# Performance work log

Measured on AMD Instinct MI355X. Metric: run time of the kernel, lower is better.

## Reference

```python
import jax, jax.numpy as jnp
import numpy as np

NUM_HEADS = 16
HIDDEN = 1024
HEAD_DIM = HIDDEN // NUM_HEADS


def setup_inputs() -> dict:
    key = jax.random.key(0)
    ks = jax.random.split(key, 12)
    B, S, H = 4, 1024, HIDDEN
    s = 1.0 / np.sqrt(H)
    inp = {
        "aspect_hidden": jax.random.normal(ks[0], (B, S, H), jnp.float32),
        "opinion_hidden": jax.random.normal(ks[1], (B, S, H), jnp.float32),
        "attention_mask": jnp.ones((B, S), jnp.int32),
        # torch nn.Linear weights are [out, in]
        "Wq": jax.random.normal(ks[2], (H, H), jnp.float32) * s,
        "bq": jnp.zeros((H,), jnp.float32),
        "Wk": jax.random.normal(ks[3], (H, H), jnp.float32) * s,
        "bk": jnp.zeros((H,), jnp.float32),
        "Wv": jax.random.normal(ks[4], (H, H), jnp.float32) * s,
        "bv": jnp.zeros((H,), jnp.float32),
        "Wo": jax.random.normal(ks[5], (H, H), jnp.float32) * s,
        "bo": jnp.zeros((H,), jnp.float32),
        # nn.Bilinear(H, H, 1): weight [1, H, H], bias [1]
        "Wbil": jax.random.normal(ks[6], (1, H, H), jnp.float32) * s,
        "bbil": jnp.zeros((1,), jnp.float32),
    }
    return inp


def reference(aspect_hidden, opinion_hidden, attention_mask,
              Wq, bq, Wk, bk, Wv, bv, Wo, bo, Wbil, bbil):
    B, Sq, H = aspect_hidden.shape
    Sk = opinion_hidden.shape[1]
    nh, hd = NUM_HEADS, HEAD_DIM
    scale = hd ** (-0.5)

    q = (aspect_hidden @ Wq.T + bq).reshape(B, Sq, nh, hd).transpose(0, 2, 1, 3)
    k = (opinion_hidden @ Wk.T + bk).reshape(B, Sk, nh, hd).transpose(0, 2, 1, 3)
    v = (opinion_hidden @ Wv.T + bv).reshape(B, Sk, nh, hd).transpose(0, 2, 1, 3)

    # bilinear span bias: span[b,s] = a[b,s] @ Wbil[0] @ o[b,s] + bbil
    span = jnp.einsum('bsh,hk,bsk->bs', aspect_hidden, Wbil[0], opinion_hidden) + bbil[0]

    # scores [B, nh, Sq, Sk] with span bias broadcast over heads and keys
    scores = jnp.einsum('bhqd,bhkd->bhqk', q, k) * scale + span[:, None, :, None]
    scores = jnp.where(attention_mask[:, None, None, :] == 0, -jnp.inf, scores)

    probs = jax.nn.softmax(scores, axis=-1)
    ctx = jnp.einsum('bhqk,bhkd->bhqd', probs, v)
    ctx = ctx.transpose(0, 2, 1, 3).reshape(B, Sq, H)
    return ctx @ Wo.T + bo
```

## Files before the change

kernel.cpp:

```cpp
#include <hip/hip_runtime.h>
#include <hip/hip_bf16.h>
#include <stdint.h>

typedef __attribute__((ext_vector_type(4))) float f32x4;
typedef __attribute__((ext_vector_type(16))) float f32x16;
typedef __attribute__((ext_vector_type(8))) short bf16x8;
typedef __attribute__((ext_vector_type(4))) unsigned int u32x4;
typedef __attribute__((ext_vector_type(2))) unsigned int u32x2;
typedef unsigned short u16;

#define GBL_AS1(p) ((const __attribute__((address_space(1))) void*)(p))
#define LDS_AS3(p) ((__attribute__((address_space(3))) void*)(p))

static __device__ __forceinline__ u16 f2bf(float f) {
  __hip_bfloat16 h = __float2bfloat16(f);
  union { __hip_bfloat16 h; u16 u; } c; c.h = h;
  return c.u;
}

__global__ __launch_bounds__(256) void fused_cast(
    const float* __restrict__ a, const float* __restrict__ o,
    const float* __restrict__ wq_, const float* __restrict__ wk_,
    const float* __restrict__ wv_, const float* __restrict__ wo_,
    const int* __restrict__ mask,
    u16* __restrict__ aB, u16* __restrict__ oB,
    u16* __restrict__ WqB, u16* __restrict__ WkB,
    u16* __restrict__ WvB, u16* __restrict__ WoB,
    int* __restrict__ flags) {
  if (blockIdx.x == 0 && threadIdx.x < 64) {
    int bb = threadIdx.x >> 4, kt = threadIdx.x & 15;
    int anyz = 0;
    for (int s = 0; s < 64; ++s) anyz |= (mask[bb * 1024 + kt * 64 + s] == 0);
    flags[threadIdx.x] = anyz;
  }
  int idx = blockIdx.x * 256 + threadIdx.x;
#pragma unroll
  for (int j = 0; j < 4; ++j) {
    int i = idx + j * 786432;
    const float* src; u16* dst; int off;
    if (i < 1048576) { src = a; dst = aB; off = i; }
    else if (i < 2097152) { src = o; dst = oB; off = i - 1048576; }
    else {
      int w = (i - 2097152) >> 18; off = (i - 2097152) & 262143;
      src = (w == 0) ? wq_ : (w == 1) ? wk_ : (w == 2) ? wv_ : wo_;
      dst = (w == 0) ? WqB : (w == 1) ? WkB : (w == 2) ? WvB : WoB;
    }
    float4 v = reinterpret_cast<const float4*>(src)[off];
    ushort4 ov;
    ov.x = f2bf(v.x); ov.y = f2bf(v.y); ov.z = f2bf(v.z); ov.w = f2bf(v.w);
    reinterpret_cast<ushort4*>(dst)[off] = ov;
  }
}

static __device__ __forceinline__ void gemm_core(const u16* __restrict__ Atile,
                                                 const u16* __restrict__ Btile,
                                                 u16* lds_a, u16* lds_b,
                                                 f32x4 acc[4][4]) {
  const int tid = threadIdx.x;
  const int lane = tid & 63;
  const int wv = tid >> 6;
  const int wm = wv >> 1, wn = wv & 1;
  const int fr = lane & 15, fq = lane >> 4;
  for (int kt = 0; kt < 32; ++kt) {
#pragma unroll
    for (int i = 0; i < 2; ++i) {
      const int cb = (wv * 2 + i) * 64;
      const int c = cb + lane;
      const int row = c >> 2;
      const int off = (c & 3) * 8;
      __builtin_amdgcn_global_load_lds(GBL_AS1(Atile + (size_t)row * 1024 + kt * 32 + off),
                                       LDS_AS3(lds_a + cb * 8), 16, 0, 0);
      __builtin_amdgcn_global_load_lds(GBL_AS1(Btile + (size_t)row * 1024 + kt * 32 + off),
                                       LDS_AS3(lds_b + cb * 8), 16, 0, 0);
    }
    __syncthreads();
    bf16x8 af[4], bfv[4];
#pragma unroll
    for (int mi = 0; mi < 4; ++mi)
      af[mi] = *(const bf16x8*)&lds_a[(wm * 64 + mi * 16 + fr) * 32 + fq * 8];
#pragma unroll
    for (int ni = 0; ni < 4; ++ni)
      bfv[ni] = *(const bf16x8*)&lds_b[(wn * 64 + ni * 16 + fr) * 32 + fq * 8];
#pragma unroll
    for (int mi = 0; mi < 4; ++mi)
#pragma unroll
      for (int ni = 0; ni < 4; ++ni)
        acc[mi][ni] = __builtin_amdgcn_mfma_f32_16x16x32_bf16(af[mi], bfv[ni], acc[mi][ni], 0, 0, 0);
    __syncthreads();
  }
}

__global__ __launch_bounds__(256) void qkv_gemm(
    const u16* __restrict__ aB, const u16* __restrict__ oB,
    const u16* __restrict__ Wq, const u16* __restrict__ Wk, const u16* __restrict__ Wv,
    const float* __restrict__ bq, const float* __restrict__ bk, const float* __restrict__ bv,
    u16* __restrict__ q_ws, u16* __restrict__ k_ws, u16* __restrict__ vt_ws) {
  __shared__ __align__(16) u16 lds_a[128 * 32];
  __shared__ __align__(16) u16 lds_b[128 * 32];
  const int mt = blockIdx.x;
  const int nt = blockIdx.y;
  const int w = nt >> 3, ntl = nt & 7;
  const u16* A = (w == 0) ? aB : oB;
  const u16* W = (w == 0) ? Wq : (w == 1) ? Wk : Wv;
  const float* bias = (w == 0) ? bq : (w == 1) ? bk : bv;
  f32x4 acc[4][4];
#pragma unroll
  for (int i = 0; i < 4; ++i)
#pragma unroll
    for (int j = 0; j < 4; ++j) acc[i][j] = (f32x4){0.f, 0.f, 0.f, 0.f};
  gemm_core(A + (size_t)mt * 128 * 1024, W + (size_t)ntl * 128 * 1024, lds_a, lds_b, acc);
  const int lane = threadIdx.x & 63, wvi = threadIdx.x >> 6;
  const int wm = wvi >> 1, wn = wvi & 1, fr = lane & 15, fq = lane >> 4;
  u16* dst01 = (w == 0) ? q_ws : k_ws;
  const float qscl = (w == 0) ? 0.18033688f : 1.0f;
#pragma unroll
  for (int mi = 0; mi < 4; ++mi)
#pragma unroll
    for (int ni = 0; ni < 4; ++ni)
#pragma unroll
      for (int r = 0; r < 4; ++r) {
        int m = mt * 128 + wm * 64 + mi * 16 + fq * 4 + r;
        int nl = ntl * 128 + wn * 64 + ni * 16 + fr;
        float v = (acc[mi][ni][r] + bias[nl]) * qscl;
        int b = m >> 10, s = m & 1023, h = nl >> 6, d = nl & 63;
        u16 u = f2bf(v);
        if (w < 2) dst01[(((size_t)(b * 16 + h)) * 1024 + s) * 64 + d] = u;
        else       vt_ws[(((size_t)(b * 16 + h)) * 64 + d) * 1024 + s] = u;
      }
}

__global__ __launch_bounds__(256, 4) void attn_kernel(
    const u16* __restrict__ q_ws, const u16* __restrict__ k_ws,
    const u16* __restrict__ vt_ws, const int* __restrict__ mask,
    const int* __restrict__ flags, u16* __restrict__ ctx_ws) {
  __shared__ __align__(16) u16 k_lds[2][64 * 64];
  __shared__ __align__(16) u16 vt_lds[2][64 * 64];
  __shared__ __align__(16) float scl_lds[4][32];
  const int bid = blockIdx.x;
  const int bh = bid & 63, qt = bid >> 6;
  const int b = bh >> 4, h = bh & 15;
  const int tid = threadIdx.x, lane = tid & 63, wv = tid >> 6;
  const int l31 = lane & 31, hi = lane >> 5;
  const u16* qbase = q_ws + (size_t)bh * 65536 + (size_t)qt * 8192;
  const u16* kbase = k_ws + (size_t)bh * 65536;
  const u16* vtbase = vt_ws + (size_t)bh * 65536;

#define STAGE_KV(kt_, buf_) do { \
    _Pragma("unroll") \
    for (int i_ = 0; i_ < 2; ++i_) { \
      int cb_ = (wv * 2 + i_) * 64; \
      int c_ = cb_ + lane; \
      int r_ = c_ >> 3; \
      int sc_ = ((c_ & 7) ^ (r_ & 7)) * 8; \
      __builtin_amdgcn_global_load_lds(GBL_AS1(kbase + (size_t)((kt_) * 64 + r_) * 64 + sc_), \
                                       LDS_AS3(&k_lds[buf_][cb_ * 8]), 16, 0, 0); \
      __builtin_amdgcn_global_load_lds(GBL_AS1(vtbase + (size_t)r_ * 1024 + (kt_) * 64 + sc_), \
                                       LDS_AS3(&vt_lds[buf_][cb_ * 8]), 16, 0, 0); \
    } \
  } while (0)

  {
    u16* qstage = &k_lds[0][0];
#pragma unroll
    for (int i_ = 0; i_ < 4; ++i_) {
      int cb_ = (wv * 4 + i_) * 64;
      int c_ = cb_ + lane;
      int r_ = c_ >> 3;
      int sc_ = ((c_ & 7) ^ (r_ & 7)) * 8;
      __builtin_amdgcn_global_load_lds(GBL_AS1(qbase + (size_t)r_ * 64 + sc_),
                                       LDS_AS3(qstage + cb_ * 8), 16, 0, 0);
    }
  }
  __syncthreads();
  bf16x8 qf[4];
  {
    int rq = wv * 32 + l31;
    const u16* qr = &k_lds[0][0] + rq * 64;
    int rx = rq & 7;
#pragma unroll
    for (int ds = 0; ds < 4; ++ds)
      qf[ds] = *(const bf16x8*)&qr[((ds * 2 + hi) ^ rx) * 8];
  }
  __syncthreads();
  STAGE_KV(0, 0);
  __syncthreads();

  f32x16 ctx0, ctx1;
#pragma unroll
  for (int z = 0; z < 16; ++z) { ctx0[z] = 0.f; ctx1[z] = 0.f; }
  float psum_half = 0.f;

  for (int kt = 0; kt < 16; ++kt) {
    const int cur = kt & 1;
    if (kt < 15) STAGE_KV(kt + 1, cur ^ 1);

    f32x16 sc[2];
#pragma unroll
    for (int kb = 0; kb < 2; ++kb) {
      f32x16 a;
#pragma unroll
      for (int z = 0; z < 16; ++z) a[z] = 0.f;
      int r = kb * 32 + l31;
      const u16* kr = &k_lds[cur][r * 64];
      int rx = r & 7;
#pragma unroll
      for (int ds = 0; ds < 4; ++ds) {
        bf16x8 kf = *(const bf16x8*)&kr[((ds * 2 + hi) ^ rx) * 8];
        a = __builtin_amdgcn_mfma_f32_32x32x16_bf16(kf, qf[ds], a, 0, 0, 0);
      }
      sc[kb] = a;
    }

    if (flags[b * 16 + kt]) {
#pragma unroll
      for (int kb = 0; kb < 2; ++kb)
#pragma unroll
        for (int r2 = 0; r2 < 16; ++r2) {
          int key = kb * 32 + (r2 & 3) + 8 * (r2 >> 2) + 4 * hi;
          if (mask[b * 1024 + kt * 64 + key] == 0) sc[kb][r2] = -30000.0f;
        }
    }

#pragma unroll
    for (int kb = 0; kb < 2; ++kb)
#pragma unroll
      for (int r2 = 0; r2 < 16; ++r2) {
        float p = __builtin_exp2f(sc[kb][r2]);
        sc[kb][r2] = p;
        psum_half += p;
      }

#pragma unroll
    for (int kb = 0; kb < 2; ++kb) {
      unsigned int w[8];
#pragma unroll
      for (int j = 0; j < 8; ++j) {
        unsigned int t;
        asm("v_cvt_pk_bf16_f32 %0, %1, %2" : "=v"(t) : "v"(sc[kb][2 * j]), "v"(sc[kb][2 * j + 1]));
        w[j] = t;
      }
      u32x2 a0 = __builtin_amdgcn_permlane32_swap(w[0], w[2], false, false);
      u32x2 a1 = __builtin_amdgcn_permlane32_swap(w[1], w[3], false, false);
      u32x2 a2 = __builtin_amdgcn_permlane32_swap(w[4], w[6], false, false);
      u32x2 a3 = __builtin_amdgcn_permlane32_swap(w[5], w[7], false, false);
      union { u32x4 u; bf16x8 b; } P0, P1;
      P0.u = (u32x4){ a0[0], a1[0], a0[1], a1[1] };
      P1.u = (u32x4){ a2[0], a3[0], a2[1], a3[1] };
#pragma unroll
      for (int db = 0; db < 2; ++db) {
        int rv = db * 32 + l31;
        const u16* vr = &vt_lds[cur][rv * 64];
        int rvx = rv & 7;
        bf16x8 v0 = *(const bf16x8*)&vr[((kb * 4 + hi) ^ rvx) * 8];
        bf16x8 v1 = *(const bf16x8*)&vr[((kb * 4 + 2 + hi) ^ rvx) * 8];
        if (db == 0) {
          ctx0 = __builtin_amdgcn_mfma_f32_32x32x16_bf16(P0.b, v0, ctx0, 0, 0, 0);
          ctx0 = __builtin_amdgcn_mfma_f32_32x32x16_bf16(P1.b, v1, ctx0, 0, 0, 0);
        } else {
          ctx1 = __builtin_amdgcn_mfma_f32_32x32x16_bf16(P0.b, v0, ctx1, 0, 0, 0);
          ctx1 = __builtin_amdgcn_mfma_f32_32x32x16_bf16(P1.b, v1, ctx1, 0, 0, 0);
        }
      }
    }
    __syncthreads();
  }

  float lrow = psum_half + __shfl_xor(psum_half, 32);
  float inv = (lrow > 0.f) ? 1.0f / lrow : 0.f;
  if (hi == 0) scl_lds[wv][l31] = inv;
  asm volatile("s_waitcnt lgkmcnt(0)" ::: "memory");
  const int sbase = qt * 128 + wv * 32;
#pragma unroll
  for (int g = 0; g < 4; ++g) {
    float4 s4 = *(const float4*)&scl_lds[wv][g * 8 + hi * 4];
    const float* sp = (const float*)&s4;
#pragma unroll
    for (int i2 = 0; i2 < 4; ++i2) {
      int s = sbase + g * 8 + hi * 4 + i2;
      size_t rowoff = ((size_t)(b * 1024 + s)) * 1024 + h * 64;
      ctx_ws[rowoff + l31]      = f2bf(ctx0[g * 4 + i2] * sp[i2]);
      ctx_ws[rowoff + 32 + l31] = f2bf(ctx1[g * 4 + i2] * sp[i2]);
    }
  }
#undef STAGE_KV
}

__global__ __launch_bounds__(256) void out_gemm(const u16* __restrict__ ctxB,
                                                const u16* __restrict__ Wo,
                                                const float* __restrict__ bo,
                                                float* __restrict__ out) {
  __shared__ __align__(16) u16 lds_a[128 * 32];
  __shared__ __align__(16) u16 lds_b[128 * 32];
  const int mt = blockIdx.x, nt = blockIdx.y;
  f32x4 acc[4][4];
#pragma unroll
  for (int i = 0; i < 4; ++i)
#pragma unroll
    for (int j = 0; j < 4; ++j) acc[i][j] = (f32x4){0.f, 0.f, 0.f, 0.f};
  gemm_core(ctxB + (size_t)mt * 128 * 1024, Wo + (size_t)nt * 128 * 1024, lds_a, lds_b, acc);
  const int lane = threadIdx.x & 63, wvi = threadIdx.x >> 6;
  const int wm = wvi >> 1, wn = wvi & 1, fr = lane & 15, fq = lane >> 4;
#pragma unroll
  for (int mi = 0; mi < 4; ++mi)
#pragma unroll
    for (int ni = 0; ni < 4; ++ni)
#pragma unroll
      for (int r = 0; r < 4; ++r) {
        int m = mt * 128 + wm * 64 + mi * 16 + fq * 4 + r;
        int n = nt * 128 + wn * 64 + ni * 16 + fr;
        out[(size_t)m * 1024 + n] = acc[mi][ni][r] + bo[n];
      }
}

extern "C" void kernel_launch(void* const* d_in, const int* in_sizes, int n_in,
                              void* d_out, int out_size, void* d_ws, size_t ws_size,
                              hipStream_t stream) {
  const float* aspect = (const float*)d_in[0];
  const float* opinion = (const float*)d_in[1];
  const int* mask = (const int*)d_in[2];
  const float* Wq = (const float*)d_in[3];
  const float* bq = (const float*)d_in[4];
  const float* Wk = (const float*)d_in[5];
  const float* bk = (const float*)d_in[6];
  const float* Wv = (const float*)d_in[7];
  const float* bv = (const float*)d_in[8];
  const float* Wo = (const float*)d_in[9];
  const float* bo = (const float*)d_in[10];
  float* out = (float*)d_out;
  char* ws = (char*)d_ws;

  const size_t MB = 1u << 20;
  u16* aB    = (u16*)(ws + 0 * MB);
  u16* oB    = (u16*)(ws + 8 * MB);
  u16* WqB   = (u16*)(ws + 16 * MB);
  u16* WkB   = (u16*)(ws + 18 * MB);
  u16* WvB   = (u16*)(ws + 20 * MB);
  u16* WoB   = (u16*)(ws + 22 * MB);
  u16* q_ws  = (u16*)(ws + 24 * MB);
  u16* k_ws  = (u16*)(ws + 32 * MB);
  u16* vt_ws = (u16*)(ws + 40 * MB);
  u16* ctx_ws= (u16*)(ws + 48 * MB);
  int* flags = (int*)(out + out_size - 64);

  fused_cast<<<3072, 256, 0, stream>>>(aspect, opinion, Wq, Wk, Wv, Wo, mask,
                                       aB, oB, WqB, WkB, WvB, WoB, flags);
  qkv_gemm<<<dim3(32, 24), 256, 0, stream>>>(aB, oB, WqB, WkB, WvB, bq, bk, bv,
                                             q_ws, k_ws, vt_ws);
  attn_kernel<<<512, 256, 0, stream>>>(q_ws, k_ws, vt_ws, mask, flags, ctx_ws);
  out_gemm<<<dim3(32, 8), 256, 0, stream>>>(ctx_ws, WoB, bo, out);
}
```

Before: 109.4 us.

## Double-buffer GEMM LDS staging, remap blocks for XCD locality, vectorize V^T stores

The shared GEMM core now uses two LDS buffers and issues the global-to-LDS loads for the next k-step before computing on the current one, so memory latency overlaps the MFMA work. The QKV and output GEMMs switch to a 1D grid with an index remap that spreads consecutive block IDs across the 8 XCDs, so blocks sharing tiles run on the same XCD and can reuse its L2. The V-transpose epilogue writes four consecutive sequence positions as one ushort4 store instead of scattered 2-byte stores. The cost is doubled LDS per block (32KB) and only one barrier per iteration between the compute and the next overwrite.

```diff
diff --git a/kernel.cpp b/kernel.cpp
--- a/kernel.cpp
+++ b/kernel.cpp
@@ -61,26 +61,35 @@
   const int wv = tid >> 6;
   const int wm = wv >> 1, wn = wv & 1;
   const int fr = lane & 15, fq = lane >> 4;
+
+#define GSTAGE(kt_, buf_) do { \
+    _Pragma("unroll") \
+    for (int i_ = 0; i_ < 2; ++i_) { \
+      const int cb_ = (wv * 2 + i_) * 64; \
+      const int c_ = cb_ + lane; \
+      const int row_ = c_ >> 2; \
+      const int off_ = (c_ & 3) * 8; \
+      __builtin_amdgcn_global_load_lds(GBL_AS1(Atile + (size_t)row_ * 1024 + (kt_) * 32 + off_), \
+                                       LDS_AS3(lds_a + (buf_) * 4096 + cb_ * 8), 16, 0, 0); \
+      __builtin_amdgcn_global_load_lds(GBL_AS1(Btile + (size_t)row_ * 1024 + (kt_) * 32 + off_), \
+                                       LDS_AS3(lds_b + (buf_) * 4096 + cb_ * 8), 16, 0, 0); \
+    } \
+  } while (0)
+
+  GSTAGE(0, 0);
+  __syncthreads();
   for (int kt = 0; kt < 32; ++kt) {
-#pragma unroll
-    for (int i = 0; i < 2; ++i) {
-      const int cb = (wv * 2 + i) * 64;
-      const int c = cb + lane;
-      const int row = c >> 2;
-      const int off = (c & 3) * 8;
-      __builtin_amdgcn_global_load_lds(GBL_AS1(Atile + (size_t)row * 1024 + kt * 32 + off),
-                                       LDS_AS3(lds_a + cb * 8), 16, 0, 0);
-      __builtin_amdgcn_global_load_lds(GBL_AS1(Btile + (size_t)row * 1024 + kt * 32 + off),
-                                       LDS_AS3(lds_b + cb * 8), 16, 0, 0);
-    }
-    __syncthreads();
+    const int cur = kt & 1;
+    if (kt < 31) GSTAGE(kt + 1, cur ^ 1);
+    const u16* la = lds_a + cur * 4096;
+    const u16* lb = lds_b + cur * 4096;
     bf16x8 af[4], bfv[4];
 #pragma unroll
     for (int mi = 0; mi < 4; ++mi)
-      af[mi] = *(const bf16x8*)&lds_a[(wm * 64 + mi * 16 + fr) * 32 + fq * 8];
+      af[mi] = *(const bf16x8*)&la[(wm * 64 + mi * 16 + fr) * 32 + fq * 8];
 #pragma unroll
     for (int ni = 0; ni < 4; ++ni)
-      bfv[ni] = *(const bf16x8*)&lds_b[(wn * 64 + ni * 16 + fr) * 32 + fq * 8];
+      bfv[ni] = *(const bf16x8*)&lb[(wn * 64 + ni * 16 + fr) * 32 + fq * 8];
 #pragma unroll
     for (int mi = 0; mi < 4; ++mi)
 #pragma unroll
@@ -88,6 +97,7 @@
         acc[mi][ni] = __builtin_amdgcn_mfma_f32_16x16x32_bf16(af[mi], bfv[ni], acc[mi][ni], 0, 0, 0);
     __syncthreads();
   }
+#undef GSTAGE
 }
 
 __global__ __launch_bounds__(256) void qkv_gemm(
@@ -95,10 +105,11 @@
     const u16* __restrict__ Wq, const u16* __restrict__ Wk, const u16* __restrict__ Wv,
     const float* __restrict__ bq, const float* __restrict__ bk, const float* __restrict__ bv,
     u16* __restrict__ q_ws, u16* __restrict__ k_ws, u16* __restrict__ vt_ws) {
-  __shared__ __align__(16) u16 lds_a[128 * 32];
-  __shared__ __align__(16) u16 lds_b[128 * 32];
-  const int mt = blockIdx.x;
-  const int nt = blockIdx.y;
+  __shared__ __align__(16) u16 lds_a[2 * 128 * 32];
+  __shared__ __align__(16) u16 lds_b[2 * 128 * 32];
+  const int bid = blockIdx.x;
+  const int wk = (bid & 7) * 96 + (bid >> 3);
+  const int mt = wk & 31, nt = wk >> 5;
   const int w = nt >> 3, ntl = nt & 7;
   const u16* A = (w == 0) ? aB : oB;
   const u16* W = (w == 0) ? Wq : (w == 1) ? Wk : Wv;
@@ -111,22 +122,39 @@
   gemm_core(A + (size_t)mt * 128 * 1024, W + (size_t)ntl * 128 * 1024, lds_a, lds_b, acc);
   const int lane = threadIdx.x & 63, wvi = threadIdx.x >> 6;
   const int wm = wvi >> 1, wn = wvi & 1, fr = lane & 15, fq = lane >> 4;
-  u16* dst01 = (w == 0) ? q_ws : k_ws;
-  const float qscl = (w == 0) ? 0.18033688f : 1.0f;
-#pragma unroll
-  for (int mi = 0; mi < 4; ++mi)
-#pragma unroll
-    for (int ni = 0; ni < 4; ++ni)
-#pragma unroll
-      for (int r = 0; r < 4; ++r) {
-        int m = mt * 128 + wm * 64 + mi * 16 + fq * 4 + r;
+  if (w < 2) {
+    u16* dst01 = (w == 0) ? q_ws : k_ws;
+    const float qscl = (w == 0) ? 0.18033688f : 1.0f;
+#pragma unroll
+    for (int mi = 0; mi < 4; ++mi)
+#pragma unroll
+      for (int ni = 0; ni < 4; ++ni)
+#pragma unroll
+        for (int r = 0; r < 4; ++r) {
+          int m = mt * 128 + wm * 64 + mi * 16 + fq * 4 + r;
+          int nl = ntl * 128 + wn * 64 + ni * 16 + fr;
+          float v = (acc[mi][ni][r] + bias[nl]) * qscl;
+          int b = m >> 10, s = m & 1023, h = nl >> 6, d = nl & 63;
+          dst01[(((size_t)(b * 16 + h)) * 1024 + s) * 64 + d] = f2bf(v);
+        }
+  } else {
+#pragma unroll
+    for (int mi = 0; mi < 4; ++mi)
+#pragma unroll
+      for (int ni = 0; ni < 4; ++ni) {
         int nl = ntl * 128 + wn * 64 + ni * 16 + fr;
-        float v = (acc[mi][ni][r] + bias[nl]) * qscl;
-        int b = m >> 10, s = m & 1023, h = nl >> 6, d = nl & 63;
-        u16 u = f2bf(v);
-        if (w < 2) dst01[(((size_t)(b * 16 + h)) * 1024 + s) * 64 + d] = u;
-        else       vt_ws[(((size_t)(b * 16 + h)) * 64 + d) * 1024 + s] = u;
-      }
+        int h = nl >> 6, d = nl & 63;
+        float bv_ = bias[nl];
+        int m0 = mt * 128 + wm * 64 + mi * 16 + fq * 4;
+        int b = m0 >> 10, s0 = m0 & 1023;
+        ushort4 o;
+        o.x = f2bf(acc[mi][ni][0] + bv_);
+        o.y = f2bf(acc[mi][ni][1] + bv_);
+        o.z = f2bf(acc[mi][ni][2] + bv_);
+        o.w = f2bf(acc[mi][ni][3] + bv_);
+        *(ushort4*)&vt_ws[(((size_t)(b * 16 + h)) * 64 + d) * 1024 + s0] = o;
+      }
+  }
 }
 
 __global__ __launch_bounds__(256, 4) void attn_kernel(
@@ -289,9 +317,11 @@
                                                 const u16* __restrict__ Wo,
                                                 const float* __restrict__ bo,
                                                 float* __restrict__ out) {
-  __shared__ __align__(16) u16 lds_a[128 * 32];
-  __shared__ __align__(16) u16 lds_b[128 * 32];
-  const int mt = blockIdx.x, nt = blockIdx.y;
+  __shared__ __align__(16) u16 lds_a[2 * 128 * 32];
+  __shared__ __align__(16) u16 lds_b[2 * 128 * 32];
+  const int bid = blockIdx.x;
+  const int wk = (bid & 7) * 32 + (bid >> 3);
+  const int mt = wk & 31, nt = wk >> 5;
   f32x4 acc[4][4];
 #pragma unroll
   for (int i = 0; i < 4; ++i)
@@ -344,8 +374,8 @@
 
   fused_cast<<<3072, 256, 0, stream>>>(aspect, opinion, Wq, Wk, Wv, Wo, mask,
                                        aB, oB, WqB, WkB, WvB, WoB, flags);
-  qkv_gemm<<<dim3(32, 24), 256, 0, stream>>>(aB, oB, WqB, WkB, WvB, bq, bk, bv,
-                                             q_ws, k_ws, vt_ws);
+  qkv_gemm<<<768, 256, 0, stream>>>(aB, oB, WqB, WkB, WvB, bq, bk, bv,
+                                    q_ws, k_ws, vt_ws);
   attn_kernel<<<512, 256, 0, stream>>>(q_ws, k_ws, vt_ws, mask, flags, ctx_ws);
-  out_gemm<<<dim3(32, 8), 256, 0, stream>>>(ctx_ws, WoB, bo, out);
-}
+  out_gemm<<<256, 256, 0, stream>>>(ctx_ws, WoB, bo, out);
+}
```

Result: slower. 130.5 us (+19.3%).

## Double GEMM K-tile to 64 with XOR-swizzled LDS and vectorized V-transpose stores

Applied to the files above, without the earlier changes.

The shared GEMM core now stages 64-wide K slices instead of 32, halving the number of barrier pairs per tile. It applies an XOR swizzle to the 16-byte chunk index on both the global-to-LDS copy and the fragment reads, to avoid LDS bank conflicts. The QKV epilogue also splits the V path to write four consecutive sequence positions as one ushort4 store into the transposed V buffer instead of scalar stores. LDS per block doubles, which could reduce how many blocks fit on a CU.

```diff
diff --git a/kernel.cpp b/kernel.cpp
--- a/kernel.cpp
+++ b/kernel.cpp
@@ -61,31 +61,38 @@
   const int wv = tid >> 6;
   const int wm = wv >> 1, wn = wv & 1;
   const int fr = lane & 15, fq = lane >> 4;
-  for (int kt = 0; kt < 32; ++kt) {
-#pragma unroll
-    for (int i = 0; i < 2; ++i) {
-      const int cb = (wv * 2 + i) * 64;
+  for (int kt = 0; kt < 16; ++kt) {
+#pragma unroll
+    for (int i_ = 0; i_ < 4; ++i_) {
+      const int cb = (wv * 4 + i_) * 64;
       const int c = cb + lane;
-      const int row = c >> 2;
-      const int off = (c & 3) * 8;
-      __builtin_amdgcn_global_load_lds(GBL_AS1(Atile + (size_t)row * 1024 + kt * 32 + off),
+      const int r = c >> 3;
+      const int sc = ((c & 7) ^ (r & 7)) * 8;
+      __builtin_amdgcn_global_load_lds(GBL_AS1(Atile + (size_t)r * 1024 + kt * 64 + sc),
                                        LDS_AS3(lds_a + cb * 8), 16, 0, 0);
-      __builtin_amdgcn_global_load_lds(GBL_AS1(Btile + (size_t)row * 1024 + kt * 32 + off),
+      __builtin_amdgcn_global_load_lds(GBL_AS1(Btile + (size_t)r * 1024 + kt * 64 + sc),
                                        LDS_AS3(lds_b + cb * 8), 16, 0, 0);
     }
     __syncthreads();
-    bf16x8 af[4], bfv[4];
-#pragma unroll
-    for (int mi = 0; mi < 4; ++mi)
-      af[mi] = *(const bf16x8*)&lds_a[(wm * 64 + mi * 16 + fr) * 32 + fq * 8];
-#pragma unroll
-    for (int ni = 0; ni < 4; ++ni)
-      bfv[ni] = *(const bf16x8*)&lds_b[(wn * 64 + ni * 16 + fr) * 32 + fq * 8];
-#pragma unroll
-    for (int mi = 0; mi < 4; ++mi)
-#pragma unroll
-      for (int ni = 0; ni < 4; ++ni)
-        acc[mi][ni] = __builtin_amdgcn_mfma_f32_16x16x32_bf16(af[mi], bfv[ni], acc[mi][ni], 0, 0, 0);
+#pragma unroll
+    for (int ks = 0; ks < 2; ++ks) {
+      bf16x8 af[4], bfv[4];
+#pragma unroll
+      for (int mi = 0; mi < 4; ++mi) {
+        int r = wm * 64 + mi * 16 + fr;
+        af[mi] = *(const bf16x8*)&lds_a[r * 64 + (((ks * 4 + fq) ^ (r & 7)) * 8)];
+      }
+#pragma unroll
+      for (int ni = 0; ni < 4; ++ni) {
+        int r = wn * 64 + ni * 16 + fr;
+        bfv[ni] = *(const bf16x8*)&lds_b[r * 64 + (((ks * 4 + fq) ^ (r & 7)) * 8)];
+      }
+#pragma unroll
+      for (int mi = 0; mi < 4; ++mi)
+#pragma unroll
+        for (int ni = 0; ni < 4; ++ni)
+          acc[mi][ni] = __builtin_amdgcn_mfma_f32_16x16x32_bf16(af[mi], bfv[ni], acc[mi][ni], 0, 0, 0);
+    }
     __syncthreads();
   }
 }
@@ -95,8 +102,8 @@
     const u16* __restrict__ Wq, const u16* __restrict__ Wk, const u16* __restrict__ Wv,
     const float* __restrict__ bq, const float* __restrict__ bk, const float* __restrict__ bv,
     u16* __restrict__ q_ws, u16* __restrict__ k_ws, u16* __restrict__ vt_ws) {
-  __shared__ __align__(16) u16 lds_a[128 * 32];
-  __shared__ __align__(16) u16 lds_b[128 * 32];
+  __shared__ __align__(16) u16 lds_a[128 * 64];
+  __shared__ __align__(16) u16 lds_b[128 * 64];
   const int mt = blockIdx.x;
   const int nt = blockIdx.y;
   const int w = nt >> 3, ntl = nt & 7;
@@ -111,22 +118,39 @@
   gemm_core(A + (size_t)mt * 128 * 1024, W + (size_t)ntl * 128 * 1024, lds_a, lds_b, acc);
   const int lane = threadIdx.x & 63, wvi = threadIdx.x >> 6;
   const int wm = wvi >> 1, wn = wvi & 1, fr = lane & 15, fq = lane >> 4;
-  u16* dst01 = (w == 0) ? q_ws : k_ws;
-  const float qscl = (w == 0) ? 0.18033688f : 1.0f;
-#pragma unroll
-  for (int mi = 0; mi < 4; ++mi)
-#pragma unroll
-    for (int ni = 0; ni < 4; ++ni)
-#pragma unroll
-      for (int r = 0; r < 4; ++r) {
-        int m = mt * 128 + wm * 64 + mi * 16 + fq * 4 + r;
+  if (w < 2) {
+    u16* dst01 = (w == 0) ? q_ws : k_ws;
+    const float qscl = (w == 0) ? 0.18033688f : 1.0f;
+#pragma unroll
+    for (int mi = 0; mi < 4; ++mi)
+#pragma unroll
+      for (int ni = 0; ni < 4; ++ni)
+#pragma unroll
+        for (int r = 0; r < 4; ++r) {
+          int m = mt * 128 + wm * 64 + mi * 16 + fq * 4 + r;
+          int nl = ntl * 128 + wn * 64 + ni * 16 + fr;
+          float v = (acc[mi][ni][r] + bias[nl]) * qscl;
+          int b = m >> 10, s = m & 1023, h = nl >> 6, d = nl & 63;
+          dst01[(((size_t)(b * 16 + h)) * 1024 + s) * 64 + d] = f2bf(v);
+        }
+  } else {
+#pragma unroll
+    for (int mi = 0; mi < 4; ++mi)
+#pragma unroll
+      for (int ni = 0; ni < 4; ++ni) {
         int nl = ntl * 128 + wn * 64 + ni * 16 + fr;
-        float v = (acc[mi][ni][r] + bias[nl]) * qscl;
-        int b = m >> 10, s = m & 1023, h = nl >> 6, d = nl & 63;
-        u16 u = f2bf(v);
-        if (w < 2) dst01[(((size_t)(b * 16 + h)) * 1024 + s) * 64 + d] = u;
-        else       vt_ws[(((size_t)(b * 16 + h)) * 64 + d) * 1024 + s] = u;
-      }
+        int h = nl >> 6, d = nl & 63;
+        float bv_ = bias[nl];
+        int m0 = mt * 128 + wm * 64 + mi * 16 + fq * 4;
+        int b = m0 >> 10, s0 = m0 & 1023;
+        ushort4 o;
+        o.x = f2bf(acc[mi][ni][0] + bv_);
+        o.y = f2bf(acc[mi][ni][1] + bv_);
+        o.z = f2bf(acc[mi][ni][2] + bv_);
+        o.w = f2bf(acc[mi][ni][3] + bv_);
+        *(ushort4*)&vt_ws[(((size_t)(b * 16 + h)) * 64 + d) * 1024 + s0] = o;
+      }
+  }
 }
 
 __global__ __launch_bounds__(256, 4) void attn_kernel(
@@ -289,8 +313,8 @@
                                                 const u16* __restrict__ Wo,
                                                 const float* __restrict__ bo,
                                                 float* __restrict__ out) {
-  __shared__ __align__(16) u16 lds_a[128 * 32];
-  __shared__ __align__(16) u16 lds_b[128 * 32];
+  __shared__ __align__(16) u16 lds_a[128 * 64];
+  __shared__ __align__(16) u16 lds_b[128 * 64];
   const int mt = blockIdx.x, nt = blockIdx.y;
   f32x4 acc[4][4];
 #pragma unroll
```

After: 111.9 us. 2.2% more time.

## Vectorize transposed V stores and stagger GEMM block start with s_sleep

Applied to the files above, without the earlier changes.

The QKV GEMM epilogue now splits the Q/K path from the V path. The transposed V^T path packs four consecutive sequence elements into one 8-byte ushort4 store instead of four scattered 2-byte stores. Both GEMM kernels also add an s_sleep delay chosen by workgroup index, so successive waves of blocks start out of phase and compete less for memory at the same moment. The sleep adds a small fixed delay to some blocks.

```diff
diff --git a/kernel.cpp b/kernel.cpp
--- a/kernel.cpp
+++ b/kernel.cpp
@@ -90,6 +90,12 @@
   }
 }
 
+static __device__ __forceinline__ void phase_stagger(int bid) {
+  int ph = (bid >> 8) % 3;
+  if (ph == 1) asm volatile("s_sleep 6");
+  else if (ph == 2) asm volatile("s_sleep 11");
+}
+
 __global__ __launch_bounds__(256) void qkv_gemm(
     const u16* __restrict__ aB, const u16* __restrict__ oB,
     const u16* __restrict__ Wq, const u16* __restrict__ Wk, const u16* __restrict__ Wv,
@@ -99,6 +105,7 @@
   __shared__ __align__(16) u16 lds_b[128 * 32];
   const int mt = blockIdx.x;
   const int nt = blockIdx.y;
+  phase_stagger(mt + nt * 32);
   const int w = nt >> 3, ntl = nt & 7;
   const u16* A = (w == 0) ? aB : oB;
   const u16* W = (w == 0) ? Wq : (w == 1) ? Wk : Wv;
@@ -111,22 +118,39 @@
   gemm_core(A + (size_t)mt * 128 * 1024, W + (size_t)ntl * 128 * 1024, lds_a, lds_b, acc);
   const int lane = threadIdx.x & 63, wvi = threadIdx.x >> 6;
   const int wm = wvi >> 1, wn = wvi & 1, fr = lane & 15, fq = lane >> 4;
-  u16* dst01 = (w == 0) ? q_ws : k_ws;
-  const float qscl = (w == 0) ? 0.18033688f : 1.0f;
-#pragma unroll
-  for (int mi = 0; mi < 4; ++mi)
-#pragma unroll
-    for (int ni = 0; ni < 4; ++ni)
-#pragma unroll
-      for (int r = 0; r < 4; ++r) {
-        int m = mt * 128 + wm * 64 + mi * 16 + fq * 4 + r;
+  if (w < 2) {
+    u16* dst01 = (w == 0) ? q_ws : k_ws;
+    const float qscl = (w == 0) ? 0.18033688f : 1.0f;
+#pragma unroll
+    for (int mi = 0; mi < 4; ++mi)
+#pragma unroll
+      for (int ni = 0; ni < 4; ++ni)
+#pragma unroll
+        for (int r = 0; r < 4; ++r) {
+          int m = mt * 128 + wm * 64 + mi * 16 + fq * 4 + r;
+          int nl = ntl * 128 + wn * 64 + ni * 16 + fr;
+          float v = (acc[mi][ni][r] + bias[nl]) * qscl;
+          int b = m >> 10, s = m & 1023, h = nl >> 6, d = nl & 63;
+          dst01[(((size_t)(b * 16 + h)) * 1024 + s) * 64 + d] = f2bf(v);
+        }
+  } else {
+#pragma unroll
+    for (int mi = 0; mi < 4; ++mi)
+#pragma unroll
+      for (int ni = 0; ni < 4; ++ni) {
         int nl = ntl * 128 + wn * 64 + ni * 16 + fr;
-        float v = (acc[mi][ni][r] + bias[nl]) * qscl;
-        int b = m >> 10, s = m & 1023, h = nl >> 6, d = nl & 63;
-        u16 u = f2bf(v);
-        if (w < 2) dst01[(((size_t)(b * 16 + h)) * 1024 + s) * 64 + d] = u;
-        else       vt_ws[(((size_t)(b * 16 + h)) * 64 + d) * 1024 + s] = u;
-      }
+        int h = nl >> 6, d = nl & 63;
+        float bv_ = bias[nl];
+        int m0 = mt * 128 + wm * 64 + mi * 16 + fq * 4;
+        int b = m0 >> 10, s0 = m0 & 1023;
+        ushort4 o;
+        o.x = f2bf(acc[mi][ni][0] + bv_);
+        o.y = f2bf(acc[mi][ni][1] + bv_);
+        o.z = f2bf(acc[mi][ni][2] + bv_);
+        o.w = f2bf(acc[mi][ni][3] + bv_);
+        *(ushort4*)&vt_ws[(((size_t)(b * 16 + h)) * 64 + d) * 1024 + s0] = o;
+      }
+  }
 }
 
 __global__ __launch_bounds__(256, 4) void attn_kernel(
@@ -292,6 +316,7 @@
   __shared__ __align__(16) u16 lds_a[128 * 32];
   __shared__ __align__(16) u16 lds_b[128 * 32];
   const int mt = blockIdx.x, nt = blockIdx.y;
+  phase_stagger(mt + nt * 32);
   f32x4 acc[4][4];
 #pragma unroll
   for (int i = 0; i < 4; ++i)
```

New measurement: 118.3 us. 8.1% more time.
